# Optimization experiments

Measured on AMD Instinct MI355X. Metric: run time of the kernel, lower is better.

The kernel has to match this reference:

```python
import jax, jax.numpy as jnp
import numpy as np

B, T, IN, H, L, OUT = 512, 365, 10, 256, 2, 20


def setup_inputs() -> dict:
    key = jax.random.key(0)
    ks = jax.random.split(key, 12)
    s = 1.0 / np.sqrt(H)
    inp = {
        "x": jax.random.normal(ks[0], (B, T, IN), dtype=jnp.float32),
        "times": jnp.arange(T, dtype=jnp.float32),
        "interpolation_method": 0,
        # layer 0 (input IN -> H); PyTorch gate order: r, z, n
        "W_ih0": jax.random.uniform(ks[1], (3 * H, IN), minval=-s, maxval=s),
        "W_hh0": jax.random.uniform(ks[2], (3 * H, H), minval=-s, maxval=s),
        "b_ih0": jax.random.uniform(ks[3], (3 * H,), minval=-s, maxval=s),
        "b_hh0": jax.random.uniform(ks[4], (3 * H,), minval=-s, maxval=s),
        # layer 1 (H -> H)
        "W_ih1": jax.random.uniform(ks[5], (3 * H, H), minval=-s, maxval=s),
        "W_hh1": jax.random.uniform(ks[6], (3 * H, H), minval=-s, maxval=s),
        "b_ih1": jax.random.uniform(ks[7], (3 * H,), minval=-s, maxval=s),
        "b_hh1": jax.random.uniform(ks[8], (3 * H,), minval=-s, maxval=s),
        # final classifier
        "W_out": jax.random.uniform(ks[9], (OUT, H), minval=-s, maxval=s),
        "b_out": jax.random.uniform(ks[10], (OUT,), minval=-s, maxval=s),
    }
    return inp


def _gru_layer(xs, W_ih, W_hh, b_ih, b_hh):
    # xs: [T, B, in] time-major. Returns (all hidden states [T,B,H], final h [B,H]).
    Hd = W_hh.shape[1]

    def step(h, x_t):
        gi = x_t @ W_ih.T + b_ih          # [B, 3H]
        gh = h @ W_hh.T + b_hh            # [B, 3H]
        i_r, i_z, i_n = jnp.split(gi, 3, axis=-1)
        h_r, h_z, h_n = jnp.split(gh, 3, axis=-1)
        r = jax.nn.sigmoid(i_r + h_r)
        z = jax.nn.sigmoid(i_z + h_z)
        n = jnp.tanh(i_n + r * h_n)
        h_new = (1.0 - z) * n + z * h
        return h_new, h_new

    h0 = jnp.zeros((xs.shape[1], Hd), dtype=xs.dtype)
    h_last, ys = jax.lax.scan(step, h0, xs)
    return ys, h_last


def reference(x, times, interpolation_method, W_ih0, W_hh0, b_ih0, b_hh0,
              W_ih1, W_hh1, b_ih1, b_hh1, W_out, b_out):
    # times / interpolation_method are accepted but unused (as in the original).
    xs = jnp.transpose(x, (1, 0, 2))                      # [T, B, IN]
    ys0, _ = _gru_layer(xs, W_ih0, W_hh0, b_ih0, b_hh0)   # [T, B, H]
    _, h_last = _gru_layer(ys0, W_ih1, W_hh1, b_ih1, b_hh1)  # [B, H] == out[:, -1, :]
    logits = h_last @ W_out.T + b_out                     # [B, OUT]
    return jax.nn.softmax(logits, axis=-1)
```

## Files before the change

### kernel.cpp

```cpp
#include <hip/hip_runtime.h>
#include <math.h>

typedef __attribute__((ext_vector_type(8))) short short8;
typedef __attribute__((ext_vector_type(4))) float floatx4;
typedef __attribute__((ext_vector_type(4))) unsigned int uintx4;
typedef unsigned short ushort_t;
typedef unsigned int uint_t;
typedef unsigned long long ull_t;

constexpr int C_B   = 512;
constexpr int C_T   = 365;
constexpr int C_IN  = 10;
constexpr int C_H   = 256;
constexpr int C_OUT = 20;

constexpr int NB  = 192;

constexpr size_t PLANE_U = 48ull * 8 * 64 * 8;
constexpr size_t US_H    = 6 * PLANE_U;
constexpr size_t HP_SZU  = 512ull * 256;
constexpr int SY_TOT = 2048;
constexpr unsigned STRIP = 12;
constexpr unsigned SPIN_MAIN = 1u << 16;
constexpr unsigned SPIN_HAND = 1u << 16;

__device__ __forceinline__ float fsig(float v)  { return 1.0f / (1.0f + __expf(-v)); }
__device__ __forceinline__ float ftanh(float v) { return 2.0f / (1.0f + __expf(-2.0f * v)) - 1.0f; }

__device__ __forceinline__ void split1(float x, ushort_t& hi, ushort_t& lo) {
    unsigned u = __float_as_uint(x);
    hi = (ushort_t)(u >> 16);
    float r = x - __uint_as_float(u & 0xffff0000u);
    lo = (ushort_t)(__float_as_uint(r) >> 16);
}

__device__ __forceinline__ uint_t packsplit(float x) {
    unsigned u = __float_as_uint(x);
    unsigned hib = u & 0xffff0000u;
    float r = x - __uint_as_float(hib);
    return hib | (__float_as_uint(r) >> 16);
}

__device__ __forceinline__ float lds_h(const ushort_t* hi, const ushort_t* lo, int idx) {
    return __uint_as_float(((unsigned)hi[idx]) << 16) + __uint_as_float(((unsigned)lo[idx]) << 16);
}

__global__ __launch_bounds__(256) void prep_pack(const float* __restrict__ Whh0,
                                                 const float* __restrict__ Wih1,
                                                 const float* __restrict__ Whh1,
                                                 ushort_t* __restrict__ PW) {
    const int blk = blockIdx.x;
    const int tid = threadIdx.x;

    if (blk == 0) {
        uint_t* SY = (uint_t*)(PW + US_H) + 4 * HP_SZU;
        for (int u = tid; u < SY_TOT; u += 256)
            __hip_atomic_store(SY + u, 0u, __ATOMIC_RELAXED, __HIP_MEMORY_SCOPE_AGENT);
    }

    const int mat = blk / 48;
    const int rem = blk % 48;
    const int g   = rem / 16;
    const int jb  = rem % 16;
    const float* S = (mat == 0) ? Whh0 : (mat == 1) ? Wih1 : Whh1;

    const int jl  = tid >> 4;
    const int kc  = tid & 15;
    const int j   = jb * 16 + jl;
    const int nt  = jb * 3 + g;

    const float* src = S + (g * 256 + j) * 256 + kc * 16;
    float f[16];
#pragma unroll
    for (int q = 0; q < 4; q++) {
        float4 v = *(const float4*)(src + q * 4);
        f[q*4+0] = v.x; f[q*4+1] = v.y; f[q*4+2] = v.z; f[q*4+3] = v.w;
    }
    ushort_t hi[16], lo[16];
#pragma unroll
    for (int e = 0; e < 16; e++) split1(f[e], hi[e], lo[e]);

    ushort_t* dhi = PW + (size_t)(mat * 2 + 0) * PLANE_U;
    ushort_t* dlo = PW + (size_t)(mat * 2 + 1) * PLANE_U;
    const int ks = kc >> 1;
#pragma unroll
    for (int hh = 0; hh < 2; hh++) {
        const int quad = (kc & 1) * 2 + hh;
        const int L    = quad * 16 + jl;
        const size_t base = ((size_t)(nt * 8 + ks)) * 512 + L * 8;
        short8 vh, vl;
#pragma unroll
        for (int e = 0; e < 8; e++) { vh[e] = (short)hi[hh*8+e]; vl[e] = (short)lo[hh*8+e]; }
        *(short8*)(dhi + base) = vh;
        *(short8*)(dlo + base) = vl;
    }
}

template<bool FAST>
__device__ __forceinline__ void stage_issue(const uint_t* __restrict__ g, uintx4 (&v)[8], int tid) {
    const int c0 = (tid & 63) * 4;
    const int r0 = tid >> 6;
#pragma unroll
    for (int rr = 0; rr < 8; rr++) {
        const uint_t* p = g + (r0 + rr * 4) * 256 + c0;
        if (FAST) {
            asm volatile("global_load_dwordx4 %0, %1, off sc0"
                         : "=&v"(v[rr]) : "v"(p));
        } else {
            ull_t q0 = __hip_atomic_load((const ull_t*)(p),
                                         __ATOMIC_RELAXED, __HIP_MEMORY_SCOPE_AGENT);
            ull_t q1 = __hip_atomic_load((const ull_t*)(p + 2),
                                         __ATOMIC_RELAXED, __HIP_MEMORY_SCOPE_AGENT);
            v[rr][0] = (uint_t)q0; v[rr][1] = (uint_t)(q0 >> 32);
            v[rr][2] = (uint_t)q1; v[rr][3] = (uint_t)(q1 >> 32);
        }
    }
    if (FAST) {
        asm volatile("s_waitcnt vmcnt(0)" ::: "memory");
        __builtin_amdgcn_sched_barrier(0);
    }
}

__device__ __forceinline__ void stage_commit(const uintx4 (&v)[8], ushort_t* s_hi, ushort_t* s_lo, int tid) {
    const int c0 = (tid & 63) * 4;
    const int r0 = tid >> 6;
#pragma unroll
    for (int rr = 0; rr < 8; rr++) {
        const int row = r0 + rr * 4;
        const uint_t u0 = v[rr][0], u1 = v[rr][1], u2 = v[rr][2], u3 = v[rr][3];
        uint2 hv, lv;
        hv.x = (u0 >> 16) | (u1 & 0xffff0000u);
        hv.y = (u2 >> 16) | (u3 & 0xffff0000u);
        lv.x = (u0 & 0xffffu) | (u1 << 16);
        lv.y = (u2 & 0xffffu) | (u3 << 16);
        *(uint2*)(s_hi + row * 264 + c0) = hv;
        *(uint2*)(s_lo + row * 264 + c0) = lv;
    }
}

template<bool FAST>
__device__ __forceinline__ void st_h(uint_t* p, uint_t val) {
    if (FAST) {
        *p = val;
    } else {
        __hip_atomic_store(p, val, __ATOMIC_RELAXED, __HIP_MEMORY_SCOPE_AGENT);
    }
}

__device__ __forceinline__ uint_t ld_flag(const uint_t* p) {
    return __hip_atomic_load(p, __ATOMIC_RELAXED, __HIP_MEMORY_SCOPE_AGENT);
}

__device__ __forceinline__ void publish(uint_t* cme) {
    __hip_atomic_fetch_add(cme, 1u, __ATOMIC_RELAXED, __HIP_MEMORY_SCOPE_AGENT);
}

__device__ __forceinline__ void wave_gemm(const ushort_t* sh_hi, const ushort_t* sh_lo,
                                          const ushort_t* __restrict__ bh_base,
                                          const ushort_t* __restrict__ bl_base,
                                          int jbg, int lane, floatx4 acc[3][2]) {
    const int m = lane & 15, quad = lane >> 4;
    const int aoff = m * 264 + quad * 8;
#pragma unroll
    for (int ks = 0; ks < 8; ks++) {
        short8 a0h = *(const short8*)(sh_hi + aoff + ks * 32);
        short8 a0l = *(const short8*)(sh_lo + aoff + ks * 32);
        short8 a1h = *(const short8*)(sh_hi + aoff + 16 * 264 + ks * 32);
        short8 a1l = *(const short8*)(sh_lo + aoff + 16 * 264 + ks * 32);
#pragma unroll
        for (int g = 0; g < 3; g++) {
            const size_t boff = (size_t)(jbg * 3 + g) * 4096 + (size_t)ks * 512 + lane * 8;
            short8 bh = *(const short8*)(bh_base + boff);
            short8 bl = *(const short8*)(bl_base + boff);
            acc[g][0] = __builtin_amdgcn_mfma_f32_16x16x32_bf16(a0h, bh, acc[g][0], 0, 0, 0);
            acc[g][0] = __builtin_amdgcn_mfma_f32_16x16x32_bf16(a0l, bh, acc[g][0], 0, 0, 0);
            acc[g][0] = __builtin_amdgcn_mfma_f32_16x16x32_bf16(a0h, bl, acc[g][0], 0, 0, 0);
            acc[g][1] = __builtin_amdgcn_mfma_f32_16x16x32_bf16(a1h, bh, acc[g][1], 0, 0, 0);
            acc[g][1] = __builtin_amdgcn_mfma_f32_16x16x32_bf16(a1l, bh, acc[g][1], 0, 0, 0);
            acc[g][1] = __builtin_amdgcn_mfma_f32_16x16x32_bf16(a1h, bl, acc[g][1], 0, 0, 0);
        }
    }
}

template<bool FAST>
__device__ __forceinline__ void gru_loop(
    const float* __restrict__ x,
    const float* __restrict__ Wih0,
    const float* __restrict__ bih0, const float* __restrict__ bhh0,
    const float* __restrict__ bih1, const float* __restrict__ bhh1,
    ushort_t* __restrict__ WS,
    int mt, int ng, bool isL0, int tid,
    ushort_t* shA_hi, ushort_t* shA_lo, ushort_t* shB_hi, ushort_t* shB_lo,
    float (*xs)[C_IN], float (*ldH)[3][32][17])
{
    const int lane = tid & 63;
    const int w    = tid >> 6;
    const int jlo  = lane & 15;
    const int quad = lane >> 4;
    const int b0   = mt * 32;

    uint_t* const hU  = (uint_t*)(WS + US_H);
    uint_t* const cme = hU + 4 * HP_SZU + mt * 32;

    const int jbg0  = ng * 4 + w;
    const int mat   = w >> 1;
    const int jbsub = w & 1;
    const int jbg1  = ng * 2 + jbsub;

    float wxr[C_IN], wxz[C_IN], wxn[C_IN];
    float b_r = 0.f, b_z = 0.f, b_in = 0.f, b_hn = 0.f;
    if (isL0) {
        const int j = jbg0 * 16 + jlo;
#pragma unroll
        for (int i = 0; i < C_IN; i++) {
            wxr[i] = Wih0[j * C_IN + i];
            wxz[i] = Wih0[(256 + j) * C_IN + i];
            wxn[i] = Wih0[(512 + j) * C_IN + i];
        }
        b_r  = bih0[j] + bhh0[j];
        b_z  = bih0[256 + j] + bhh0[256 + j];
        b_in = bih0[512 + j];
        b_hn = bhh0[512 + j];
    } else if (mat == 0) {
        const int j = jbg1 * 16 + jlo;
        b_r  = bih1[j] + bhh1[j];
        b_z  = bih1[256 + j] + bhh1[256 + j];
        b_in = bih1[512 + j];
        b_hn = bhh1[512 + j];
    }
    const int rA = tid / C_IN, cA = tid - rA * C_IN;
    const int uB = tid + 256;
    const int rB = uB / C_IN, cB = uB - rB * C_IN;
    const int xoffA = (b0 + rA) * (C_T * C_IN) + cA;
    const int xoffB = (b0 + rB) * (C_T * C_IN) + cB;

#pragma unroll 1
    for (int k = 0; k <= C_T; ++k) {
        const int srcp = (k + 1) & 1, dstp = k & 1;
        const bool do_l0 = isL0 && (k < C_T);
        const bool l0z   = (k == 0);
        const bool do_l1 = (!isL0) && (k >= 1);
        const bool l1z   = (k == 1);

        float xa = 0.f, xb = 0.f;
        if (do_l0) {
            xa = x[xoffA + k * C_IN];
            if (tid < 64) xb = x[xoffB + k * C_IN];
        }

        if (k > 0) {
            const uint_t tgt = STRIP * (uint_t)k;
            uint_t it = 0;
            while (ld_flag(cme) < tgt) {
                if (++it > SPIN_MAIN) break;
                __builtin_amdgcn_s_sleep(1);
            }
        }

        if (isL0) {
            if (do_l0) {
                xs[rA][cA] = xa;
                if (tid < 64) xs[rB][cB] = xb;
                if (!l0z) {
                    uintx4 va[8];
                    const uint_t* h0sb = hU + (size_t)srcp * HP_SZU + b0 * 256;
                    stage_issue<FAST>(h0sb, va, tid);
                    stage_commit(va, shA_hi, shA_lo, tid);
                }
                __syncthreads();

                floatx4 acc[3][2];
#pragma unroll
                for (int g = 0; g < 3; g++) { acc[g][0] = (floatx4){0,0,0,0}; acc[g][1] = (floatx4){0,0,0,0}; }
                if (!l0z)
                    wave_gemm(shA_hi, shA_lo, WS, WS + PLANE_U, jbg0, lane, acc);

                uint_t* const h0d = hU + (size_t)dstp * HP_SZU;
                const int j = jbg0 * 16 + jlo;
#pragma unroll
                for (int m = 0; m < 2; m++) {
#pragma unroll
                    for (int r = 0; r < 4; r++) {
                        const int row = m * 16 + quad * 4 + r;
                        float xrv = 0.f, xzv = 0.f, xnv = 0.f;
#pragma unroll
                        for (int i = 0; i < C_IN; i++) {
                            const float xv = xs[row][i];
                            xrv += xv * wxr[i]; xzv += xv * wxz[i]; xnv += xv * wxn[i];
                        }
                        const int gi = (b0 + row) * C_H + j;
                        const float hp = l0z ? 0.f : lds_h(shA_hi, shA_lo, row * 264 + j);
                        const float ar  = acc[0][m][r] + xrv + b_r;
                        const float az  = acc[1][m][r] + xzv + b_z;
                        const float inn = xnv + b_in;
                        const float hn  = acc[2][m][r] + b_hn;
                        const float rg = fsig(ar), zg = fsig(az);
                        const float nn = ftanh(inn + rg * hn);
                        st_h<FAST>(h0d + gi, packsplit(zg * (hp - nn) + nn));
                    }
                }
            }
        } else {
            if (do_l1) {
                uintx4 va[8], vb[8];
                const uint_t* h0sb = hU + (size_t)srcp * HP_SZU + b0 * 256;
                const uint_t* h1sb = hU + (size_t)(2 + srcp) * HP_SZU + b0 * 256;
                stage_issue<FAST>(h0sb, va, tid);
                stage_commit(va, shA_hi, shA_lo, tid);
                if (!l1z) {
                    stage_issue<FAST>(h1sb, vb, tid);
                    stage_commit(vb, shB_hi, shB_lo, tid);
                }
                __syncthreads();

                floatx4 acc[3][2];
#pragma unroll
                for (int g = 0; g < 3; g++) { acc[g][0] = (floatx4){0,0,0,0}; acc[g][1] = (floatx4){0,0,0,0}; }
                if (mat == 0)
                    wave_gemm(shA_hi, shA_lo, WS + 2 * PLANE_U, WS + 3 * PLANE_U, jbg1, lane, acc);
                else if (!l1z)
                    wave_gemm(shB_hi, shB_lo, WS + 4 * PLANE_U, WS + 5 * PLANE_U, jbg1, lane, acc);

                if (mat == 1) {
#pragma unroll
                    for (int g = 0; g < 3; g++)
#pragma unroll
                        for (int m = 0; m < 2; m++)
#pragma unroll
                            for (int r = 0; r < 4; r++)
                                ldH[jbsub][g][m * 16 + quad * 4 + r][jlo] = acc[g][m][r];
                }
                __syncthreads();

                if (mat == 0) {
                    const int j = jbg1 * 16 + jlo;
                    uint_t* const h1d = hU + (size_t)(2 + dstp) * HP_SZU;
#pragma unroll
                    for (int m = 0; m < 2; m++) {
#pragma unroll
                        for (int r = 0; r < 4; r++) {
                            const int row = m * 16 + quad * 4 + r;
                            const int gi = (b0 + row) * C_H + j;
                            const float hp = l1z ? 0.f : lds_h(shB_hi, shB_lo, row * 264 + j);
                            const float ar  = acc[0][m][r] + ldH[jbsub][0][row][jlo] + b_r;
                            const float az  = acc[1][m][r] + ldH[jbsub][1][row][jlo] + b_z;
                            const float inn = acc[2][m][r] + b_in;
                            const float hn  = ldH[jbsub][2][row][jlo] + b_hn;
                            const float rg = fsig(ar), zg = fsig(az);
                            const float nn = ftanh(inn + rg * hn);
                            st_h<FAST>(h1d + gi, packsplit(zg * (hp - nn) + nn));
                        }
                    }
                }
            }
        }

        __syncthreads();
        if (tid == 0) publish(cme);
    }
}

__global__ __launch_bounds__(256) void gru_persistent(
    const float* __restrict__ x,
    const float* __restrict__ Wih0,
    const float* __restrict__ bih0, const float* __restrict__ bhh0,
    const float* __restrict__ bih1, const float* __restrict__ bhh1,
    ushort_t* __restrict__ WS)
{
    __shared__ __align__(16) ushort_t shA_hi[32 * 264], shA_lo[32 * 264];
    __shared__ __align__(16) ushort_t shB_hi[32 * 264], shB_lo[32 * 264];
    __shared__ float xs[32][C_IN];
    __shared__ float ldH[2][3][32][17];
    __shared__ int fastFlag;

    const int tid = threadIdx.x;
    const int bid = blockIdx.x;
    const int slot = bid >> 3;
    const int mt   = (bid & 7) + ((slot >= 12) ? 8 : 0);
    const int role = (slot >= 12) ? slot - 12 : slot;
    const bool isL0 = role < 4;
    const int ng = isL0 ? role : role - 4;

    uint_t* const hU  = (uint_t*)(WS + US_H);
    uint_t* const SY  = hU + 4 * HP_SZU;
    uint_t* const rdy = SY + 512 + mt * 32;
    uint_t* const xct = SY + 1024 + mt * 32;

    if (tid == 0) {
        uint_t xcc;
        asm volatile("s_getreg_b32 %0, hwreg(HW_REG_XCC_ID)" : "=s"(xcc));
        __hip_atomic_store(xct + role, xcc | 0x100u, __ATOMIC_RELAXED, __HIP_MEMORY_SCOPE_AGENT);
        __hip_atomic_fetch_add(rdy, 1u, __ATOMIC_RELEASE, __HIP_MEMORY_SCOPE_AGENT);
        uint_t it = 0;
        while (__hip_atomic_load(rdy, __ATOMIC_RELAXED, __HIP_MEMORY_SCOPE_AGENT) < STRIP) {
            if (++it > SPIN_HAND) break;
            __builtin_amdgcn_s_sleep(8);
        }
        int ok = 1;
        const uint_t me = xcc | 0x100u;
        for (int r2 = 0; r2 < 12; r2++) {
            uint_t v = __hip_atomic_load(xct + r2, __ATOMIC_RELAXED, __HIP_MEMORY_SCOPE_AGENT);
            if (v != me) ok = 0;
        }
        fastFlag = ok;
    }
    __syncthreads();
    const bool fast = (fastFlag != 0);

    if (fast)
        gru_loop<true >(x, Wih0, bih0, bhh0, bih1, bhh1, WS, mt, ng, isL0, tid,
                        shA_hi, shA_lo, shB_hi, shB_lo, xs, ldH);
    else
        gru_loop<false>(x, Wih0, bih0, bhh0, bih1, bhh1, WS, mt, ng, isL0, tid,
                        shA_hi, shA_lo, shB_hi, shB_lo, xs, ldH);
}

__global__ __launch_bounds__(256) void classifier_kernel(
    const ushort_t* __restrict__ WS,
    const float* __restrict__ Wout, const float* __restrict__ bout,
    float* __restrict__ out)
{
    __shared__ float hs[32][C_H + 4];
    __shared__ float lg[32 * C_OUT];
    const int tid = threadIdx.x;
    const int b0  = blockIdx.x * 32;
    const uint_t* hp1 = (const uint_t*)(WS + US_H) + 3 * HP_SZU;
#pragma unroll
    for (int i = 0; i < 32; i++) {
        uint_t u = hp1[(b0 + i) * C_H + tid];
        hs[i][tid] = __uint_as_float(u & 0xffff0000u) + __uint_as_float(u << 16);
    }
    __syncthreads();
    for (int u = tid; u < 32 * C_OUT; u += 256) {
        int bb = u / C_OUT, o = u - bb * C_OUT;
        const float* wr = Wout + o * C_H;
        float acc = bout[o];
#pragma unroll 4
        for (int k = 0; k < C_H; k += 4) {
            float4 wv = *(const float4*)(wr + k);
            float4 hv = *(const float4*)(&hs[bb][k]);
            acc += wv.x*hv.x + wv.y*hv.y + wv.z*hv.z + wv.w*hv.w;
        }
        lg[u] = acc;
    }
    __syncthreads();
    if (tid < 32) {
        float mx = -1e30f;
#pragma unroll
        for (int o = 0; o < C_OUT; o++) mx = fmaxf(mx, lg[tid * C_OUT + o]);
        float e[C_OUT];
        float s = 0.0f;
#pragma unroll
        for (int o = 0; o < C_OUT; o++) { e[o] = __expf(lg[tid * C_OUT + o] - mx); s += e[o]; }
        float inv = 1.0f / s;
#pragma unroll
        for (int o = 0; o < C_OUT; o++) out[(b0 + tid) * C_OUT + o] = e[o] * inv;
    }
}

extern "C" void kernel_launch(void* const* d_in, const int* in_sizes, int n_in,
                              void* d_out, int out_size, void* d_ws, size_t ws_size,
                              hipStream_t stream) {
    const float* x    = (const float*)d_in[0];
    const float* Wih0 = (const float*)d_in[3];
    const float* Whh0 = (const float*)d_in[4];
    const float* bih0 = (const float*)d_in[5];
    const float* bhh0 = (const float*)d_in[6];
    const float* Wih1 = (const float*)d_in[7];
    const float* Whh1 = (const float*)d_in[8];
    const float* bih1 = (const float*)d_in[9];
    const float* bhh1 = (const float*)d_in[10];
    const float* Wout = (const float*)d_in[11];
    const float* bout = (const float*)d_in[12];
    float* out = (float*)d_out;
    ushort_t* WS = (ushort_t*)d_ws;

    prep_pack<<<144, 256, 0, stream>>>(Whh0, Wih1, Whh1, WS);
    gru_persistent<<<NB, 256, 0, stream>>>(x, Wih0, bih0, bhh0, bih1, bhh1, WS);
    classifier_kernel<<<C_B / 32, 256, 0, stream>>>(WS, Wout, bout, out);
}
```

Measured before the change: 2.843 ms.

## Fuse layer-0 and layer-1 work into every block, dropping role split

Instead of dedicated layer-0 and layer-1 blocks (12 per batch strip, 192 total), each of 128 blocks now computes both layers for a 32-column slice. Every wave handles one 16-row m-tile across three weight matrices, which removes the LDS exchange of hidden-hidden partials and the extra barrier. The cost is more per-block work per step and fewer blocks, with a shorter spin limit. The classifier now reads the final hidden state from the other parity buffer to match the changed timestep indexing.

```diff
diff --git a/kernel.cpp b/kernel.cpp
--- a/kernel.cpp
+++ b/kernel.cpp
@@ -14,14 +14,14 @@
 constexpr int C_H   = 256;
 constexpr int C_OUT = 20;
 
-constexpr int NB  = 192;
+constexpr int NB  = 128;
 
 constexpr size_t PLANE_U = 48ull * 8 * 64 * 8;
 constexpr size_t US_H    = 6 * PLANE_U;
 constexpr size_t HP_SZU  = 512ull * 256;
 constexpr int SY_TOT = 2048;
-constexpr unsigned STRIP = 12;
-constexpr unsigned SPIN_MAIN = 1u << 16;
+constexpr unsigned STRIP = 8;
+constexpr unsigned SPIN_MAIN = 1u << 14;
 constexpr unsigned SPIN_HAND = 1u << 16;
 
 __device__ __forceinline__ float fsig(float v)  { return 1.0f / (1.0f + __expf(-v)); }
@@ -150,34 +150,27 @@
 __device__ __forceinline__ uint_t ld_flag(const uint_t* p) {
     return __hip_atomic_load(p, __ATOMIC_RELAXED, __HIP_MEMORY_SCOPE_AGENT);
 }
-
 __device__ __forceinline__ void publish(uint_t* cme) {
     __hip_atomic_fetch_add(cme, 1u, __ATOMIC_RELAXED, __HIP_MEMORY_SCOPE_AGENT);
 }
 
-__device__ __forceinline__ void wave_gemm(const ushort_t* sh_hi, const ushort_t* sh_lo,
-                                          const ushort_t* __restrict__ bh_base,
-                                          const ushort_t* __restrict__ bl_base,
-                                          int jbg, int lane, floatx4 acc[3][2]) {
-    const int m = lane & 15, quad = lane >> 4;
-    const int aoff = m * 264 + quad * 8;
+__device__ __forceinline__ void wave_gemm1(const ushort_t* shh, const ushort_t* shl,
+                                           const ushort_t* __restrict__ bh_base,
+                                           const ushort_t* __restrict__ bl_base,
+                                           int jbg, int lane, int aoff,
+                                           floatx4 (&acc)[3]) {
 #pragma unroll
     for (int ks = 0; ks < 8; ks++) {
-        short8 a0h = *(const short8*)(sh_hi + aoff + ks * 32);
-        short8 a0l = *(const short8*)(sh_lo + aoff + ks * 32);
-        short8 a1h = *(const short8*)(sh_hi + aoff + 16 * 264 + ks * 32);
-        short8 a1l = *(const short8*)(sh_lo + aoff + 16 * 264 + ks * 32);
+        short8 ah = *(const short8*)(shh + aoff + ks * 32);
+        short8 al = *(const short8*)(shl + aoff + ks * 32);
 #pragma unroll
         for (int g = 0; g < 3; g++) {
             const size_t boff = (size_t)(jbg * 3 + g) * 4096 + (size_t)ks * 512 + lane * 8;
             short8 bh = *(const short8*)(bh_base + boff);
             short8 bl = *(const short8*)(bl_base + boff);
-            acc[g][0] = __builtin_amdgcn_mfma_f32_16x16x32_bf16(a0h, bh, acc[g][0], 0, 0, 0);
-            acc[g][0] = __builtin_amdgcn_mfma_f32_16x16x32_bf16(a0l, bh, acc[g][0], 0, 0, 0);
-            acc[g][0] = __builtin_amdgcn_mfma_f32_16x16x32_bf16(a0h, bl, acc[g][0], 0, 0, 0);
-            acc[g][1] = __builtin_amdgcn_mfma_f32_16x16x32_bf16(a1h, bh, acc[g][1], 0, 0, 0);
-            acc[g][1] = __builtin_amdgcn_mfma_f32_16x16x32_bf16(a1l, bh, acc[g][1], 0, 0, 0);
-            acc[g][1] = __builtin_amdgcn_mfma_f32_16x16x32_bf16(a1h, bl, acc[g][1], 0, 0, 0);
+            acc[g] = __builtin_amdgcn_mfma_f32_16x16x32_bf16(ah, bh, acc[g], 0, 0, 0);
+            acc[g] = __builtin_amdgcn_mfma_f32_16x16x32_bf16(al, bh, acc[g], 0, 0, 0);
+            acc[g] = __builtin_amdgcn_mfma_f32_16x16x32_bf16(ah, bl, acc[g], 0, 0, 0);
         }
     }
 }
@@ -189,45 +182,44 @@
     const float* __restrict__ bih0, const float* __restrict__ bhh0,
     const float* __restrict__ bih1, const float* __restrict__ bhh1,
     ushort_t* __restrict__ WS,
-    int mt, int ng, bool isL0, int tid,
-    ushort_t* shA_hi, ushort_t* shA_lo, ushort_t* shB_hi, ushort_t* shB_lo,
-    float (*xs)[C_IN], float (*ldH)[3][32][17])
+    int mt, int ng, int tid,
+    ushort_t* sAh, ushort_t* sAl, ushort_t* sBh, ushort_t* sBl,
+    float (*xs)[C_IN])
 {
-    const int lane = tid & 63;
-    const int w    = tid >> 6;
-    const int jlo  = lane & 15;
-    const int quad = lane >> 4;
-    const int b0   = mt * 32;
+    const int lane  = tid & 63;
+    const int w     = tid >> 6;
+    const int jlo   = lane & 15;
+    const int quad  = lane >> 4;
+    const int b0    = mt * 32;
+    const int mtile = w & 1;
+    const int jbg   = ng * 2 + (w >> 1);
+    const int j     = jbg * 16 + jlo;
 
     uint_t* const hU  = (uint_t*)(WS + US_H);
     uint_t* const cme = hU + 4 * HP_SZU + mt * 32;
 
-    const int jbg0  = ng * 4 + w;
-    const int mat   = w >> 1;
-    const int jbsub = w & 1;
-    const int jbg1  = ng * 2 + jbsub;
+    const ushort_t* W0h = WS;                const ushort_t* W0l = WS + PLANE_U;
+    const ushort_t* W1h = WS + 2 * PLANE_U;  const ushort_t* W1l = WS + 3 * PLANE_U;
+    const ushort_t* W2h = WS + 4 * PLANE_U;  const ushort_t* W2l = WS + 5 * PLANE_U;
 
     float wxr[C_IN], wxz[C_IN], wxn[C_IN];
-    float b_r = 0.f, b_z = 0.f, b_in = 0.f, b_hn = 0.f;
-    if (isL0) {
-        const int j = jbg0 * 16 + jlo;
-#pragma unroll
-        for (int i = 0; i < C_IN; i++) {
-            wxr[i] = Wih0[j * C_IN + i];
-            wxz[i] = Wih0[(256 + j) * C_IN + i];
-            wxn[i] = Wih0[(512 + j) * C_IN + i];
-        }
-        b_r  = bih0[j] + bhh0[j];
-        b_z  = bih0[256 + j] + bhh0[256 + j];
-        b_in = bih0[512 + j];
-        b_hn = bhh0[512 + j];
-    } else if (mat == 0) {
-        const int j = jbg1 * 16 + jlo;
-        b_r  = bih1[j] + bhh1[j];
-        b_z  = bih1[256 + j] + bhh1[256 + j];
-        b_in = bih1[512 + j];
-        b_hn = bhh1[512 + j];
-    }
+#pragma unroll
+    for (int i = 0; i < C_IN; i++) {
+        wxr[i] = Wih0[j * C_IN + i];
+        wxz[i] = Wih0[(256 + j) * C_IN + i];
+        wxn[i] = Wih0[(512 + j) * C_IN + i];
+    }
+    const float b_r  = bih0[j] + bhh0[j];
+    const float b_z  = bih0[256 + j] + bhh0[256 + j];
+    const float b_i0 = bih0[512 + j];
+    const float b_h0 = bhh0[512 + j];
+    const float cbr  = bih1[j] + bhh1[j];
+    const float cbz  = bih1[256 + j] + bhh1[256 + j];
+    const float cbi  = bih1[512 + j];
+    const float cbh  = bhh1[512 + j];
+
+    const int aoff = jlo * 264 + quad * 8 + mtile * (16 * 264);
+
     const int rA = tid / C_IN, cA = tid - rA * C_IN;
     const int uB = tid + 256;
     const int rB = uB / C_IN, cB = uB - rB * C_IN;
@@ -236,14 +228,10 @@
 
 #pragma unroll 1
     for (int k = 0; k <= C_T; ++k) {
-        const int srcp = (k + 1) & 1, dstp = k & 1;
-        const bool do_l0 = isL0 && (k < C_T);
-        const bool l0z   = (k == 0);
-        const bool do_l1 = (!isL0) && (k >= 1);
-        const bool l1z   = (k == 1);
+        const bool do0 = (k < C_T);
 
         float xa = 0.f, xb = 0.f;
-        if (do_l0) {
+        if (do0) {
             xa = x[xoffA + k * C_IN];
             if (tid < 64) xb = x[xoffB + k * C_IN];
         }
@@ -257,101 +245,69 @@
             }
         }
 
-        if (isL0) {
-            if (do_l0) {
-                xs[rA][cA] = xa;
-                if (tid < 64) xs[rB][cB] = xb;
-                if (!l0z) {
-                    uintx4 va[8];
-                    const uint_t* h0sb = hU + (size_t)srcp * HP_SZU + b0 * 256;
-                    stage_issue<FAST>(h0sb, va, tid);
-                    stage_commit(va, shA_hi, shA_lo, tid);
+        if (k >= 1) {
+            uintx4 va[8];
+            const uint_t* h0sb = hU + (size_t)((k + 1) & 1) * HP_SZU + b0 * 256;
+            stage_issue<FAST>(h0sb, va, tid);
+            stage_commit(va, sAh, sAl, tid);
+        }
+        if (k >= 2) {
+            uintx4 vb[8];
+            const uint_t* h1sb = hU + (size_t)(2 + (k & 1)) * HP_SZU + b0 * 256;
+            stage_issue<FAST>(h1sb, vb, tid);
+            stage_commit(vb, sBh, sBl, tid);
+        }
+        if (do0) {
+            xs[rA][cA] = xa;
+            if (tid < 64) xs[rB][cB] = xb;
+        }
+        __syncthreads();
+
+        floatx4 a0[3], aA[3], aB[3];
+#pragma unroll
+        for (int g = 0; g < 3; g++) {
+            a0[g] = (floatx4){0,0,0,0}; aA[g] = (floatx4){0,0,0,0}; aB[g] = (floatx4){0,0,0,0};
+        }
+        if (do0 && k >= 1) wave_gemm1(sAh, sAl, W0h, W0l, jbg, lane, aoff, a0);
+        if (k >= 1)        wave_gemm1(sAh, sAl, W1h, W1l, jbg, lane, aoff, aA);
+        if (k >= 2)        wave_gemm1(sBh, sBl, W2h, W2l, jbg, lane, aoff, aB);
+
+        if (do0) {
+            uint_t* const h0d = hU + (size_t)(k & 1) * HP_SZU;
+#pragma unroll
+            for (int r = 0; r < 4; r++) {
+                const int row = mtile * 16 + quad * 4 + r;
+                float xrv = 0.f, xzv = 0.f, xnv = 0.f;
+#pragma unroll
+                for (int i = 0; i < C_IN; i++) {
+                    const float xvv = xs[row][i];
+                    xrv += xvv * wxr[i]; xzv += xvv * wxz[i]; xnv += xvv * wxn[i];
                 }
-                __syncthreads();
-
-                floatx4 acc[3][2];
-#pragma unroll
-                for (int g = 0; g < 3; g++) { acc[g][0] = (floatx4){0,0,0,0}; acc[g][1] = (floatx4){0,0,0,0}; }
-                if (!l0z)
-                    wave_gemm(shA_hi, shA_lo, WS, WS + PLANE_U, jbg0, lane, acc);
-
-                uint_t* const h0d = hU + (size_t)dstp * HP_SZU;
-                const int j = jbg0 * 16 + jlo;
-#pragma unroll
-                for (int m = 0; m < 2; m++) {
-#pragma unroll
-                    for (int r = 0; r < 4; r++) {
-                        const int row = m * 16 + quad * 4 + r;
-                        float xrv = 0.f, xzv = 0.f, xnv = 0.f;
-#pragma unroll
-                        for (int i = 0; i < C_IN; i++) {
-                            const float xv = xs[row][i];
-                            xrv += xv * wxr[i]; xzv += xv * wxz[i]; xnv += xv * wxn[i];
-                        }
-                        const int gi = (b0 + row) * C_H + j;
-                        const float hp = l0z ? 0.f : lds_h(shA_hi, shA_lo, row * 264 + j);
-                        const float ar  = acc[0][m][r] + xrv + b_r;
-                        const float az  = acc[1][m][r] + xzv + b_z;
-                        const float inn = xnv + b_in;
-                        const float hn  = acc[2][m][r] + b_hn;
-                        const float rg = fsig(ar), zg = fsig(az);
-                        const float nn = ftanh(inn + rg * hn);
-                        st_h<FAST>(h0d + gi, packsplit(zg * (hp - nn) + nn));
-                    }
-                }
+                const int gi = (b0 + row) * C_H + j;
+                const float hp = (k >= 1) ? lds_h(sAh, sAl, row * 264 + j) : 0.f;
+                const float ar  = a0[0][r] + xrv + b_r;
+                const float az  = a0[1][r] + xzv + b_z;
+                const float inn = xnv + b_i0;
+                const float hn  = a0[2][r] + b_h0;
+                const float rg = fsig(ar), zg = fsig(az);
+                const float nn = ftanh(inn + rg * hn);
+                st_h<FAST>(h0d + gi, packsplit(zg * (hp - nn) + nn));
             }
-        } else {
-            if (do_l1) {
-                uintx4 va[8], vb[8];
-                const uint_t* h0sb = hU + (size_t)srcp * HP_SZU + b0 * 256;
-                const uint_t* h1sb = hU + (size_t)(2 + srcp) * HP_SZU + b0 * 256;
-                stage_issue<FAST>(h0sb, va, tid);
-                stage_commit(va, shA_hi, shA_lo, tid);
-                if (!l1z) {
-                    stage_issue<FAST>(h1sb, vb, tid);
-                    stage_commit(vb, shB_hi, shB_lo, tid);
-                }
-                __syncthreads();
-
-                floatx4 acc[3][2];
-#pragma unroll
-                for (int g = 0; g < 3; g++) { acc[g][0] = (floatx4){0,0,0,0}; acc[g][1] = (floatx4){0,0,0,0}; }
-                if (mat == 0)
-                    wave_gemm(shA_hi, shA_lo, WS + 2 * PLANE_U, WS + 3 * PLANE_U, jbg1, lane, acc);
-                else if (!l1z)
-                    wave_gemm(shB_hi, shB_lo, WS + 4 * PLANE_U, WS + 5 * PLANE_U, jbg1, lane, acc);
-
-                if (mat == 1) {
-#pragma unroll
-                    for (int g = 0; g < 3; g++)
-#pragma unroll
-                        for (int m = 0; m < 2; m++)
-#pragma unroll
-                            for (int r = 0; r < 4; r++)
-                                ldH[jbsub][g][m * 16 + quad * 4 + r][jlo] = acc[g][m][r];
-                }
-                __syncthreads();
-
-                if (mat == 0) {
-                    const int j = jbg1 * 16 + jlo;
-                    uint_t* const h1d = hU + (size_t)(2 + dstp) * HP_SZU;
-#pragma unroll
-                    for (int m = 0; m < 2; m++) {
-#pragma unroll
-                        for (int r = 0; r < 4; r++) {
-                            const int row = m * 16 + quad * 4 + r;
-                            const int gi = (b0 + row) * C_H + j;
-                            const float hp = l1z ? 0.f : lds_h(shB_hi, shB_lo, row * 264 + j);
-                            const float ar  = acc[0][m][r] + ldH[jbsub][0][row][jlo] + b_r;
-                            const float az  = acc[1][m][r] + ldH[jbsub][1][row][jlo] + b_z;
-                            const float inn = acc[2][m][r] + b_in;
-                            const float hn  = ldH[jbsub][2][row][jlo] + b_hn;
-                            const float rg = fsig(ar), zg = fsig(az);
-                            const float nn = ftanh(inn + rg * hn);
-                            st_h<FAST>(h1d + gi, packsplit(zg * (hp - nn) + nn));
-                        }
-                    }
-                }
+        }
+        if (k >= 1) {
+            uint_t* const h1d = hU + (size_t)(2 + ((k - 1) & 1)) * HP_SZU;
+#pragma unroll
+            for (int r = 0; r < 4; r++) {
+                const int row = mtile * 16 + quad * 4 + r;
+                const int gi = (b0 + row) * C_H + j;
+                const float hp = (k >= 2) ? lds_h(sBh, sBl, row * 264 + j) : 0.f;
+                const float ar  = aA[0][r] + aB[0][r] + cbr;
+                const float az  = aA[1][r] + aB[1][r] + cbz;
+                const float inn = aA[2][r] + cbi;
+                const float hn  = aB[2][r] + cbh;
+                const float rg = fsig(ar), zg = fsig(az);
+                const float nn = ftanh(inn + rg * hn);
+                st_h<FAST>(h1d + gi, packsplit(zg * (hp - nn) + nn));
             }
         }
 
@@ -367,19 +323,15 @@
     const float* __restrict__ bih1, const float* __restrict__ bhh1,
     ushort_t* __restrict__ WS)
 {
-    __shared__ __align__(16) ushort_t shA_hi[32 * 264], shA_lo[32 * 264];
-    __shared__ __align__(16) ushort_t shB_hi[32 * 264], shB_lo[32 * 264];
+    __shared__ __align__(16) ushort_t sAh[32 * 264], sAl[32 * 264];
+    __shared__ __align__(16) ushort_t sBh[32 * 264], sBl[32 * 264];
     __shared__ float xs[32][C_IN];
-    __shared__ float ldH[2][3][32][17];
     __shared__ int fastFlag;
 
     const int tid = threadIdx.x;
     const int bid = blockIdx.x;
-    const int slot = bid >> 3;
-    const int mt   = (bid & 7) + ((slot >= 12) ? 8 : 0);
-    const int role = (slot >= 12) ? slot - 12 : slot;
-    const bool isL0 = role < 4;
-    const int ng = isL0 ? role : role - 4;
+    const int mt = (bid & 7) + ((bid >= 64) ? 8 : 0);
+    const int ng = (bid >> 3) & 7;
 
     uint_t* const hU  = (uint_t*)(WS + US_H);
     uint_t* const SY  = hU + 4 * HP_SZU;
@@ -389,7 +341,7 @@
     if (tid == 0) {
         uint_t xcc;
         asm volatile("s_getreg_b32 %0, hwreg(HW_REG_XCC_ID)" : "=s"(xcc));
-        __hip_atomic_store(xct + role, xcc | 0x100u, __ATOMIC_RELAXED, __HIP_MEMORY_SCOPE_AGENT);
+        __hip_atomic_store(xct + ng, xcc | 0x100u, __ATOMIC_RELAXED, __HIP_MEMORY_SCOPE_AGENT);
         __hip_atomic_fetch_add(rdy, 1u, __ATOMIC_RELEASE, __HIP_MEMORY_SCOPE_AGENT);
         uint_t it = 0;
         while (__hip_atomic_load(rdy, __ATOMIC_RELAXED, __HIP_MEMORY_SCOPE_AGENT) < STRIP) {
@@ -398,7 +350,7 @@
         }
         int ok = 1;
         const uint_t me = xcc | 0x100u;
-        for (int r2 = 0; r2 < 12; r2++) {
+        for (int r2 = 0; r2 < (int)STRIP; r2++) {
             uint_t v = __hip_atomic_load(xct + r2, __ATOMIC_RELAXED, __HIP_MEMORY_SCOPE_AGENT);
             if (v != me) ok = 0;
         }
@@ -408,11 +360,11 @@
     const bool fast = (fastFlag != 0);
 
     if (fast)
-        gru_loop<true >(x, Wih0, bih0, bhh0, bih1, bhh1, WS, mt, ng, isL0, tid,
-                        shA_hi, shA_lo, shB_hi, shB_lo, xs, ldH);
+        gru_loop<true >(x, Wih0, bih0, bhh0, bih1, bhh1, WS, mt, ng, tid,
+                        sAh, sAl, sBh, sBl, xs);
     else
-        gru_loop<false>(x, Wih0, bih0, bhh0, bih1, bhh1, WS, mt, ng, isL0, tid,
-                        shA_hi, shA_lo, shB_hi, shB_lo, xs, ldH);
+        gru_loop<false>(x, Wih0, bih0, bhh0, bih1, bhh1, WS, mt, ng, tid,
+                        sAh, sAl, sBh, sBl, xs);
 }
 
 __global__ __launch_bounds__(256) void classifier_kernel(
@@ -424,7 +376,7 @@
     __shared__ float lg[32 * C_OUT];
     const int tid = threadIdx.x;
     const int b0  = blockIdx.x * 32;
-    const uint_t* hp1 = (const uint_t*)(WS + US_H) + 3 * HP_SZU;
+    const uint_t* hp1 = (const uint_t*)(WS + US_H) + 2 * HP_SZU;
 #pragma unroll
     for (int i = 0; i < 32; i++) {
         uint_t u = hp1[(b0 + i) * C_H + tid];
```

New measurement: 4.402 ms. 1.55x slower.

## Split per-strip step counter into separate layer-0 and layer-1 counters with triple buffering

Applied to the files above, without the earlier changes.

Replaces the single per-strip barrier counter, which all 12 blocks incremented every step, with two counters: one published by the layer-0 blocks and one by the layer-1 blocks. The layer-0 hidden state moves from double to triple buffering, so layer 0 can run up to one step ahead of layer 1 and each layer waits only on the producers it actually depends on. This loosens the lock-step coupling between the two layers and lets their work overlap. The spin timeout is also reduced, which makes a silent break out of the wait loop, and a possible race, more likely if a wait runs long. The workspace grows by one hidden-state plane.

```diff
diff --git a/kernel.cpp b/kernel.cpp
--- a/kernel.cpp
+++ b/kernel.cpp
@@ -14,6 +14,7 @@
 constexpr int C_H   = 256;
 constexpr int C_OUT = 20;
 
+constexpr int L0B = 64;
 constexpr int NB  = 192;
 
 constexpr size_t PLANE_U = 48ull * 8 * 64 * 8;
@@ -21,7 +22,7 @@
 constexpr size_t HP_SZU  = 512ull * 256;
 constexpr int SY_TOT = 2048;
 constexpr unsigned STRIP = 12;
-constexpr unsigned SPIN_MAIN = 1u << 16;
+constexpr unsigned SPIN_MAIN = 4096;
 constexpr unsigned SPIN_HAND = 1u << 16;
 
 __device__ __forceinline__ float fsig(float v)  { return 1.0f / (1.0f + __expf(-v)); }
@@ -53,7 +54,7 @@
     const int tid = threadIdx.x;
 
     if (blk == 0) {
-        uint_t* SY = (uint_t*)(PW + US_H) + 4 * HP_SZU;
+        uint_t* SY = (uint_t*)(PW + US_H) + 5 * HP_SZU;
         for (int u = tid; u < SY_TOT; u += 256)
             __hip_atomic_store(SY + u, 0u, __ATOMIC_RELAXED, __HIP_MEMORY_SCOPE_AGENT);
     }
@@ -147,10 +148,13 @@
     }
 }
 
-__device__ __forceinline__ uint_t ld_flag(const uint_t* p) {
-    return __hip_atomic_load(p, __ATOMIC_RELAXED, __HIP_MEMORY_SCOPE_AGENT);
-}
-
+__device__ __forceinline__ void spin_ge(const uint_t* p, uint_t tgt) {
+    uint_t it = 0;
+    while (__hip_atomic_load(p, __ATOMIC_RELAXED, __HIP_MEMORY_SCOPE_AGENT) < tgt) {
+        if (++it > SPIN_MAIN) break;
+        __builtin_amdgcn_s_sleep(1);
+    }
+}
 __device__ __forceinline__ void publish(uint_t* cme) {
     __hip_atomic_fetch_add(cme, 1u, __ATOMIC_RELAXED, __HIP_MEMORY_SCOPE_AGENT);
 }
@@ -199,8 +203,9 @@
     const int quad = lane >> 4;
     const int b0   = mt * 32;
 
-    uint_t* const hU  = (uint_t*)(WS + US_H);
-    uint_t* const cme = hU + 4 * HP_SZU + mt * 32;
+    uint_t* const hU = (uint_t*)(WS + US_H);
+    uint_t* const c0 = hU + 5 * HP_SZU + mt * 32;
+    uint_t* const c1 = c0 + 512;
 
     const int jbg0  = ng * 4 + w;
     const int mat   = w >> 1;
@@ -236,7 +241,6 @@
 
 #pragma unroll 1
     for (int k = 0; k <= C_T; ++k) {
-        const int srcp = (k + 1) & 1, dstp = k & 1;
         const bool do_l0 = isL0 && (k < C_T);
         const bool l0z   = (k == 0);
         const bool do_l1 = (!isL0) && (k >= 1);
@@ -248,13 +252,12 @@
             if (tid < 64) xb = x[xoffB + k * C_IN];
         }
 
-        if (k > 0) {
-            const uint_t tgt = STRIP * (uint_t)k;
-            uint_t it = 0;
-            while (ld_flag(cme) < tgt) {
-                if (++it > SPIN_MAIN) break;
-                __builtin_amdgcn_s_sleep(1);
-            }
+        if (isL0) {
+            if (k >= 1) spin_ge(c0, 4u * (uint_t)k);
+            if (k >= 3) spin_ge(c1, 8u * (uint_t)(k - 1));
+        } else {
+            if (k >= 1) spin_ge(c0, 4u * (uint_t)k);
+            if (k >= 2) spin_ge(c1, 8u * (uint_t)k);
         }
 
         if (isL0) {
@@ -263,7 +266,7 @@
                 if (tid < 64) xs[rB][cB] = xb;
                 if (!l0z) {
                     uintx4 va[8];
-                    const uint_t* h0sb = hU + (size_t)srcp * HP_SZU + b0 * 256;
+                    const uint_t* h0sb = hU + (size_t)((k - 1) % 3) * HP_SZU + b0 * 256;
                     stage_issue<FAST>(h0sb, va, tid);
                     stage_commit(va, shA_hi, shA_lo, tid);
                 }
@@ -275,7 +278,7 @@
                 if (!l0z)
                     wave_gemm(shA_hi, shA_lo, WS, WS + PLANE_U, jbg0, lane, acc);
 
-                uint_t* const h0d = hU + (size_t)dstp * HP_SZU;
+                uint_t* const h0d = hU + (size_t)(k % 3) * HP_SZU;
                 const int j = jbg0 * 16 + jlo;
 #pragma unroll
                 for (int m = 0; m < 2; m++) {
@@ -285,8 +288,8 @@
                         float xrv = 0.f, xzv = 0.f, xnv = 0.f;
 #pragma unroll
                         for (int i = 0; i < C_IN; i++) {
-                            const float xv = xs[row][i];
-                            xrv += xv * wxr[i]; xzv += xv * wxz[i]; xnv += xv * wxn[i];
+                            const float xvv = xs[row][i];
+                            xrv += xvv * wxr[i]; xzv += xvv * wxz[i]; xnv += xvv * wxn[i];
                         }
                         const int gi = (b0 + row) * C_H + j;
                         const float hp = l0z ? 0.f : lds_h(shA_hi, shA_lo, row * 264 + j);
@@ -303,11 +306,11 @@
         } else {
             if (do_l1) {
                 uintx4 va[8], vb[8];
-                const uint_t* h0sb = hU + (size_t)srcp * HP_SZU + b0 * 256;
-                const uint_t* h1sb = hU + (size_t)(2 + srcp) * HP_SZU + b0 * 256;
+                const uint_t* h0sb = hU + (size_t)((k - 1) % 3) * HP_SZU + b0 * 256;
                 stage_issue<FAST>(h0sb, va, tid);
                 stage_commit(va, shA_hi, shA_lo, tid);
                 if (!l1z) {
+                    const uint_t* h1sb = hU + (size_t)(3 + (k & 1)) * HP_SZU + b0 * 256;
                     stage_issue<FAST>(h1sb, vb, tid);
                     stage_commit(vb, shB_hi, shB_lo, tid);
                 }
@@ -334,7 +337,7 @@
 
                 if (mat == 0) {
                     const int j = jbg1 * 16 + jlo;
-                    uint_t* const h1d = hU + (size_t)(2 + dstp) * HP_SZU;
+                    uint_t* const h1d = hU + (size_t)(3 + ((k - 1) & 1)) * HP_SZU;
 #pragma unroll
                     for (int m = 0; m < 2; m++) {
 #pragma unroll
@@ -356,7 +359,7 @@
         }
 
         __syncthreads();
-        if (tid == 0) publish(cme);
+        if (tid == 0) publish(isL0 ? c0 : c1);
     }
 }
 
@@ -382,9 +385,9 @@
     const int ng = isL0 ? role : role - 4;
 
     uint_t* const hU  = (uint_t*)(WS + US_H);
-    uint_t* const SY  = hU + 4 * HP_SZU;
-    uint_t* const rdy = SY + 512 + mt * 32;
-    uint_t* const xct = SY + 1024 + mt * 32;
+    uint_t* const SY  = hU + 5 * HP_SZU;
+    uint_t* const rdy = SY + 1024 + mt * 32;
+    uint_t* const xct = SY + 1536 + mt * 32;
 
     if (tid == 0) {
         uint_t xcc;
@@ -398,7 +401,7 @@
         }
         int ok = 1;
         const uint_t me = xcc | 0x100u;
-        for (int r2 = 0; r2 < 12; r2++) {
+        for (int r2 = 0; r2 < (int)STRIP; r2++) {
             uint_t v = __hip_atomic_load(xct + r2, __ATOMIC_RELAXED, __HIP_MEMORY_SCOPE_AGENT);
             if (v != me) ok = 0;
         }
```

Result: faster. 2.701 ms (-5.0%).
